# Kernel optimization log

Measured on AMD Instinct MI355X. Metric: run time of the kernel, lower is better.

The kernel has to match this reference:

```python
import jax, jax.numpy as jnp
import numpy as np

B, S, DIN = 4, 1024, 256      # batch, seq_len, input feature dim
KD, V = 64, 256               # keys, values
H, T = 8, 4                   # heads, stacks
EPS = 1e-3                    # keras BatchNormalization default epsilon


def setup_inputs() -> dict:
    key = jax.random.key(0)
    ks = jax.random.split(key, 6)
    def he(k, shape, fan_in):
        return jax.random.normal(k, shape, jnp.float32) * np.float32(np.sqrt(2.0 / fan_in))
    return {
        "x": jax.random.normal(ks[0], (B, S, DIN), jnp.float32),
        "W_in": he(ks[1], (DIN, V), DIN),
        "Wq": he(ks[2], (H, T, V, KD), V),
        "Wk": he(ks[3], (H, T, V, KD), V),
        "Wv": he(ks[4], (H, T, V, V), V),
        "Wd": he(ks[5], (H, T, V, V), V),
        "gamma1": jnp.ones((H, T, V), jnp.float32),
        "beta1": jnp.zeros((H, T, V), jnp.float32),
        "gamma2": jnp.ones((H, T, V), jnp.float32),
        "beta2": jnp.zeros((H, T, V), jnp.float32),
    }


def _bn(x, g, b):
    # Keras BatchNormalization(axis=-1), training-mode batch statistics over (B, S)
    m = jnp.mean(x, axis=(0, 1), keepdims=True)
    v = jnp.var(x, axis=(0, 1), keepdims=True)
    return (x - m) * jax.lax.rsqrt(v + EPS) * g + b


def reference(x, W_in, Wq, Wk, Wv, Wd, gamma1, beta1, gamma2, beta2):
    net0 = jnp.einsum('bsd,dv->bsv', x, W_in)          # input_dense, no bias
    scale = KD ** -0.5

    def one_head(Wq_h, Wk_h, Wv_h, Wd_h, g1, b1, g2, b2):
        net = net0
        for t in range(T):  # small fixed stack count, structurally distinct params
            q = net @ Wq_h[t]                           # [B,S,KD]
            k = net @ Wk_h[t]                           # [B,S,KD]
            v = net @ Wv_h[t]                           # [B,S,V]
            attn = jax.nn.softmax(jnp.einsum('bik,bjk->bij', q, k) * scale, axis=-1)
            out = jnp.einsum('bij,bjv->biv', attn, v)   # [B,S,V]
            net = _bn(net + out, g1[t], b1[t])          # residual + norm1
            net = _bn(net + jax.nn.relu(net @ Wd_h[t]), g2[t], b2[t])  # res + dense-relu + norm2
        return net                                      # [B,S,V]

    outs = jax.vmap(one_head)(Wq, Wk, Wv, Wd, gamma1, beta1, gamma2, beta2)  # [H,B,S,V]
    return jnp.transpose(outs, (1, 2, 0, 3))            # stack axis=2 -> [B,S,H,V]
```

## Files before the change

### kernel.cpp

```cpp
#include <hip/hip_runtime.h>
#include <hip/hip_bf16.h>
#include <math.h>

#define BB   4
#define SS   1024
#define VV   256
#define KDIM 64
#define HH   8
#define TT   4
#define EPSV 1e-3f
#define SCL  0.125f
#define INV2048 4.8828125e-4f

typedef float f4 __attribute__((ext_vector_type(4)));
typedef short bf8 __attribute__((ext_vector_type(8)));
typedef _Float16 h8 __attribute__((ext_vector_type(8)));
typedef _Float16 h4 __attribute__((ext_vector_type(4)));

#define LDP 68
#define LHS 68

__device__ __forceinline__ short f2bf(float x) {
  __hip_bfloat16 h = __float2bfloat16(x);
  return *reinterpret_cast<short*>(&h);
}
__device__ __forceinline__ float bf2f(short h) {
  union { unsigned u; float f; } cv;
  cv.u = ((unsigned)(unsigned short)h) << 16;
  return cv.f;
}

__device__ __forceinline__ int xcd_swz512(int L) {
  return (L & 7) * 64 + (L >> 3);
}

__global__ __launch_bounds__(256) void k_init(float* __restrict__ g, float* __restrict__ b)
{
  int i = blockIdx.x * 256 + threadIdx.x;
  g[i] = 1.f; b[i] = 0.f;
}

__global__ __launch_bounds__(256) void k_affine(
    const float* __restrict__ st, const float* __restrict__ gamma,
    const float* __restrict__ beta, int t,
    float* __restrict__ ag, float* __restrict__ ab)
{
  int h = blockIdx.x, c = threadIdx.x;
  float s  = st[(h * 256 + c) * 2];
  float s2 = st[(h * 256 + c) * 2 + 1];
  float mean = s * (1.f / 4096.f);
  float var  = s2 * (1.f / 4096.f) - mean * mean;
  float g = gamma[(h * TT + t) * 256 + c] * rsqrtf(var + EPSV);
  ag[h * 256 + c] = g;
  ab[h * 256 + c] = beta[(h * TT + t) * 256 + c] - mean * g;
}

__device__ __forceinline__ void gemm_core(
    const float* __restrict__ A, const float* __restrict__ Bm, int ldb,
    float acc[4][4], float (*As)[LDP], float (*Bs)[LDP])
{
  const int tid = threadIdx.x;
  const int tx = tid & 15, ty = tid >> 4;
#pragma unroll
  for (int i = 0; i < 4; i++)
#pragma unroll
    for (int j = 0; j < 4; j++) acc[i][j] = 0.f;

  for (int k0 = 0; k0 < 256; k0 += 16) {
#pragma unroll
    for (int l = 0; l < 4; l++) {
      int e = tid + l * 256;
      int r = e >> 4, kk = e & 15;
      As[kk][r] = A[r * 256 + k0 + kk];
      int rb = e >> 6, nn = e & 63;
      Bs[rb][nn] = Bm[(k0 + rb) * ldb + nn];
    }
    __syncthreads();
#pragma unroll
    for (int kk = 0; kk < 16; kk++) {
      f4 av = *(const f4*)&As[kk][ty * 4];
      f4 bv = *(const f4*)&Bs[kk][tx * 4];
#pragma unroll
      for (int i = 0; i < 4; i++)
#pragma unroll
        for (int j = 0; j < 4; j++)
          acc[i][j] += av[i] * bv[j];
    }
    __syncthreads();
  }
}

__global__ __launch_bounds__(256) void k_in_dense(
    const float* __restrict__ x, const float* __restrict__ Win,
    float* __restrict__ net)
{
  __shared__ __align__(16) float As[16][LDP];
  __shared__ __align__(16) float Bs[16][LDP];
  const int mt = blockIdx.x, nt = blockIdx.y;
  float acc[4][4];
  gemm_core(x + mt * 64 * 256, Win + nt * 64, 256, acc, As, Bs);
  const int tx = threadIdx.x & 15, ty = threadIdx.x >> 4;
#pragma unroll
  for (int i = 0; i < 4; i++) {
    f4 v;
#pragma unroll
    for (int j = 0; j < 4; j++) v[j] = acc[i][j];
    int row = mt * 64 + ty * 4 + i;
    int col = nt * 64 + tx * 4;
    for (int h = 0; h < HH; h++)
      *(f4*)&net[(size_t)h * 1048576 + row * 256 + col] = v;
  }
}

__global__ __launch_bounds__(256) void k_prep(
    const float* __restrict__ Wq, const float* __restrict__ Wk,
    const float* __restrict__ Wv, const float* __restrict__ Wd,
    _Float16* __restrict__ oh, _Float16* __restrict__ ol, int t)
{
  __shared__ __align__(16) _Float16 Th[64][LHS];
  __shared__ __align__(16) _Float16 Tl[64][LHS];
  const int xb = blockIdx.x, kb = blockIdx.y, h = blockIdx.z;
  const int tid = threadIdx.x;
  const float* src; int N, nb; size_t dbase;
  if (xb == 0)      { src = Wq; N = 64;  nb = 0;      dbase = (size_t)h * 16384; }
  else if (xb == 1) { src = Wk; N = 64;  nb = 0;      dbase = 131072 + (size_t)h * 16384; }
  else if (xb < 6)  { src = Wv; N = 256; nb = xb - 2; dbase = 262144 + (size_t)h * 65536; }
  else              { src = Wd; N = 256; nb = xb - 6; dbase = 786432 + (size_t)h * 65536; }
  src += (size_t)(h * TT + t) * 256 * N;
#pragma unroll
  for (int i = 0; i < 4; i++) {
    int fi = tid + i * 256;
    int r = fi >> 4, c4 = fi & 15;
    f4 w = *(const f4*)&src[(size_t)(kb * 64 + r) * N + nb * 64 + c4 * 4];
    h4 hv, lv;
#pragma unroll
    for (int j = 0; j < 4; j++) {
      _Float16 hi = (_Float16)w[j];
      hv[j] = hi;
      lv[j] = (_Float16)((w[j] - (float)hi) * 2048.f);
    }
    *(h4*)&Th[r][c4 * 4] = hv;
    *(h4*)&Tl[r][c4 * 4] = lv;
  }
  __syncthreads();
#pragma unroll
  for (int i = 0; i < 4; i++) {
    int fo = tid + i * 256;
    int nr = fo >> 4, k4 = fo & 15;
    h4 hv, lv;
#pragma unroll
    for (int j = 0; j < 4; j++) { hv[j] = Th[k4 * 4 + j][nr]; lv[j] = Tl[k4 * 4 + j][nr]; }
    size_t d = dbase + (size_t)(nb * 64 + nr) * 256 + kb * 64 + k4 * 4;
    *(h4*)&oh[d] = hv;
    *(h4*)&ol[d] = lv;
  }
}

__device__ __forceinline__ void stage_issue_aff(
    const float* __restrict__ A, const float* __restrict__ ag,
    const float* __restrict__ ab, int kc, int tid, f4 w[4])
{
#pragma unroll
  for (int i = 0; i < 4; i++) {
    int fi = tid + i * 256;
    int r = fi >> 4, c4 = fi & 15;
    f4 raw = *(const f4*)&A[(size_t)r * 256 + kc * 64 + c4 * 4];
    f4 g = *(const f4*)&ag[kc * 64 + c4 * 4];
    f4 b = *(const f4*)&ab[kc * 64 + c4 * 4];
#pragma unroll
    for (int j = 0; j < 4; j++) w[i][j] = fmaf(raw[j], g[j], b[j]);
  }
}
__device__ __forceinline__ void stage_write(
    const f4 w[4], int tid, _Float16 (*Ah)[LHS], _Float16 (*Al)[LHS])
{
#pragma unroll
  for (int i = 0; i < 4; i++) {
    int fi = tid + i * 256;
    int r = fi >> 4, c4 = fi & 15;
    h4 hv, lv;
#pragma unroll
    for (int j = 0; j < 4; j++) {
      _Float16 hi = (_Float16)w[i][j];
      hv[j] = hi;
      lv[j] = (_Float16)((w[i][j] - (float)hi) * 2048.f);
    }
    *(h4*)&Ah[r][c4 * 4] = hv;
    *(h4*)&Al[r][c4 * 4] = lv;
  }
}

__global__ __launch_bounds__(256) void k_mm_qkv(
    const float* __restrict__ net,
    const float* __restrict__ affg, const float* __restrict__ affb,
    const _Float16* __restrict__ wph, const _Float16* __restrict__ wpl,
    _Float16* __restrict__ qph, _Float16* __restrict__ qpl,
    _Float16* __restrict__ kph, _Float16* __restrict__ kpl,
    short* __restrict__ vth, short* __restrict__ vtl)
{
  __shared__ __align__(16) _Float16 Ah[2][64][LHS];
  __shared__ __align__(16) _Float16 Al[2][64][LHS];
  const int logical = xcd_swz512(blockIdx.x);
  const int mt = logical & 63, h = logical >> 6;
  const int tid = threadIdx.x, wv = tid >> 6, lane = tid & 63;
  const int ln = lane & 15, quad = lane >> 4;
  const float* A = net + (size_t)h * 1048576 + (size_t)mt * 64 * 256;
  const float* ag = affg + h * 256;
  const float* ab = affb + h * 256;

  for (int half = 0; half < 2; half++) {
    size_t bb[3];
#pragma unroll
    for (int j = 0; j < 3; j++) {
      int nt = half * 3 + j;
      if (nt == 0)      bb[j] = (size_t)h * 16384;
      else if (nt == 1) bb[j] = 131072 + (size_t)h * 16384;
      else              bb[j] = 262144 + (size_t)h * 65536 + (size_t)(nt - 2) * 16384;
      bb[j] += (size_t)(wv * 16 + ln) * 256;
    }

    f4 mn[3][4], cr[3][4];
#pragma unroll
    for (int j = 0; j < 3; j++)
#pragma unroll
      for (int mf = 0; mf < 4; mf++) {
        mn[j][mf] = (f4){0.f, 0.f, 0.f, 0.f};
        cr[j][mf] = (f4){0.f, 0.f, 0.f, 0.f};
      }

    f4 w[4];
    stage_issue_aff(A, ag, ab, 0, tid, w);
    stage_write(w, tid, Ah[0], Al[0]);
    __syncthreads();

    for (int kc = 0; kc < 4; kc++) {
      const int buf = kc & 1;
      if (kc < 3) stage_issue_aff(A, ag, ab, kc + 1, tid, w);
#pragma unroll
      for (int j = 0; j < 3; j++) {
        const _Float16* bh = wph + bb[j] + kc * 64;
        const _Float16* bl = wpl + bb[j] + kc * 64;
        h8 bh0 = *(const h8*)&bh[quad * 8];
        h8 bh1 = *(const h8*)&bh[32 + quad * 8];
        h8 bl0 = *(const h8*)&bl[quad * 8];
        h8 bl1 = *(const h8*)&bl[32 + quad * 8];
#pragma unroll
        for (int mf = 0; mf < 4; mf++) {
          h8 ah0 = *(const h8*)&Ah[buf][mf * 16 + ln][quad * 8];
          h8 ah1 = *(const h8*)&Ah[buf][mf * 16 + ln][32 + quad * 8];
          h8 al0 = *(const h8*)&Al[buf][mf * 16 + ln][quad * 8];
          h8 al1 = *(const h8*)&Al[buf][mf * 16 + ln][32 + quad * 8];
          mn[j][mf] = __builtin_amdgcn_mfma_f32_16x16x32_f16(ah0, bh0, mn[j][mf], 0, 0, 0);
          mn[j][mf] = __builtin_amdgcn_mfma_f32_16x16x32_f16(ah1, bh1, mn[j][mf], 0, 0, 0);
          cr[j][mf] = __builtin_amdgcn_mfma_f32_16x16x32_f16(ah0, bl0, cr[j][mf], 0, 0, 0);
          cr[j][mf] = __builtin_amdgcn_mfma_f32_16x16x32_f16(ah1, bl1, cr[j][mf], 0, 0, 0);
          cr[j][mf] = __builtin_amdgcn_mfma_f32_16x16x32_f16(al0, bh0, cr[j][mf], 0, 0, 0);
          cr[j][mf] = __builtin_amdgcn_mfma_f32_16x16x32_f16(al1, bh1, cr[j][mf], 0, 0, 0);
        }
      }
      if (kc < 3) stage_write(w, tid, Ah[buf ^ 1], Al[buf ^ 1]);
      __syncthreads();
    }

#pragma unroll
    for (int j = 0; j < 3; j++) {
      int nt = half * 3 + j;
      if (nt <= 1) {
        _Float16* dh = (nt == 0) ? qph : kph;
        _Float16* dl = (nt == 0) ? qpl : kpl;
        int col = wv * 16 + ln;
#pragma unroll
        for (int mf = 0; mf < 4; mf++)
#pragma unroll
          for (int r = 0; r < 4; r++) {
            int row = mt * 64 + mf * 16 + quad * 4 + r;
            int b_ = row >> 10, sI = row & 1023;
            float v = mn[j][mf][r] + cr[j][mf][r] * INV2048;
            _Float16 hi = (_Float16)v;
            size_t idx = ((size_t)(h * 4 + b_) * 1024 + sI) * 64 + col;
            dh[idx] = hi;
            dl[idx] = (_Float16)((v - (float)hi) * 2048.f);
          }
      } else {
        int c = (nt - 2) * 64 + wv * 16 + ln;
#pragma unroll
        for (int mf = 0; mf < 4; mf++)
#pragma unroll
          for (int r = 0; r < 4; r++) {
            int row = mt * 64 + mf * 16 + quad * 4 + r;
            int b_ = row >> 10, sI = row & 1023;
            float v = mn[j][mf][r] + cr[j][mf][r] * INV2048;
            short hi = f2bf(v);
            size_t idx = ((size_t)(h * 4 + b_) * 256 + c) * 1024 + sI;
            vth[idx] = hi;
            vtl[idx] = f2bf(v - bf2f(hi));
          }
      }
    }
  }
}

__global__ __launch_bounds__(256) void k_mm_dense(
    const float* __restrict__ buf1,
    const float* __restrict__ affg, const float* __restrict__ affb,
    const _Float16* __restrict__ wph, const _Float16* __restrict__ wpl,
    float* __restrict__ buf2, float* __restrict__ st)
{
  __shared__ __align__(16) _Float16 Ah[2][64][LHS];
  __shared__ __align__(16) _Float16 Al[2][64][LHS];
  const int logical = xcd_swz512(blockIdx.x);
  const int mt = logical & 63, h = logical >> 6;
  const int tid = threadIdx.x, wv = tid >> 6, lane = tid & 63;
  const int ln = lane & 15, quad = lane >> 4;
  const float* a1 = buf1 + (size_t)h * 1048576;
  float* o2 = buf2 + (size_t)h * 1048576;
  const float* A = a1 + (size_t)mt * 64 * 256;
  const float* ag = affg + h * 256;
  const float* ab = affb + h * 256;

  for (int half = 0; half < 2; half++) {
    size_t bb[2];
#pragma unroll
    for (int j = 0; j < 2; j++) {
      int nt = half * 2 + j;
      bb[j] = 786432 + (size_t)h * 65536 + (size_t)nt * 16384
            + (size_t)(wv * 16 + ln) * 256;
    }

    f4 mn[2][4], cr[2][4];
#pragma unroll
    for (int j = 0; j < 2; j++)
#pragma unroll
      for (int mf = 0; mf < 4; mf++) {
        mn[j][mf] = (f4){0.f, 0.f, 0.f, 0.f};
        cr[j][mf] = (f4){0.f, 0.f, 0.f, 0.f};
      }

    f4 w[4];
    stage_issue_aff(A, ag, ab, 0, tid, w);
    stage_write(w, tid, Ah[0], Al[0]);
    __syncthreads();

    for (int kc = 0; kc < 4; kc++) {
      const int buf = kc & 1;
      if (kc < 3) stage_issue_aff(A, ag, ab, kc + 1, tid, w);
#pragma unroll
      for (int j = 0; j < 2; j++) {
        const _Float16* bh = wph + bb[j] + kc * 64;
        const _Float16* bl = wpl + bb[j] + kc * 64;
        h8 bh0 = *(const h8*)&bh[quad * 8];
        h8 bh1 = *(const h8*)&bh[32 + quad * 8];
        h8 bl0 = *(const h8*)&bl[quad * 8];
        h8 bl1 = *(const h8*)&bl[32 + quad * 8];
#pragma unroll
        for (int mf = 0; mf < 4; mf++) {
          h8 ah0 = *(const h8*)&Ah[buf][mf * 16 + ln][quad * 8];
          h8 ah1 = *(const h8*)&Ah[buf][mf * 16 + ln][32 + quad * 8];
          h8 al0 = *(const h8*)&Al[buf][mf * 16 + ln][quad * 8];
          h8 al1 = *(const h8*)&Al[buf][mf * 16 + ln][32 + quad * 8];
          mn[j][mf] = __builtin_amdgcn_mfma_f32_16x16x32_f16(ah0, bh0, mn[j][mf], 0, 0, 0);
          mn[j][mf] = __builtin_amdgcn_mfma_f32_16x16x32_f16(ah1, bh1, mn[j][mf], 0, 0, 0);
          cr[j][mf] = __builtin_amdgcn_mfma_f32_16x16x32_f16(ah0, bl0, cr[j][mf], 0, 0, 0);
          cr[j][mf] = __builtin_amdgcn_mfma_f32_16x16x32_f16(ah1, bl1, cr[j][mf], 0, 0, 0);
          cr[j][mf] = __builtin_amdgcn_mfma_f32_16x16x32_f16(al0, bh0, cr[j][mf], 0, 0, 0);
          cr[j][mf] = __builtin_amdgcn_mfma_f32_16x16x32_f16(al1, bh1, cr[j][mf], 0, 0, 0);
        }
      }
      if (kc < 3) stage_write(w, tid, Ah[buf ^ 1], Al[buf ^ 1]);
      __syncthreads();
    }

#pragma unroll
    for (int j = 0; j < 2; j++) {
      int nt = half * 2 + j;
      int col = nt * 64 + wv * 16 + ln;
      float gc = ag[col], bc = ab[col];
      float s1 = 0.f, s2 = 0.f;
#pragma unroll
      for (int mf = 0; mf < 4; mf++)
#pragma unroll
        for (int r = 0; r < 4; r++) {
          int row = mt * 64 + mf * 16 + quad * 4 + r;
          size_t idx = (size_t)row * 256 + col;
          float v = mn[j][mf][r] + cr[j][mf][r] * INV2048;
          float yv = fmaf(a1[idx], gc, bc) + fmaxf(v, 0.f);
          o2[idx] = yv;
          s1 += yv; s2 += yv * yv;
        }
      s1 += __shfl_xor(s1, 16, 64); s1 += __shfl_xor(s1, 32, 64);
      s2 += __shfl_xor(s2, 16, 64); s2 += __shfl_xor(s2, 32, 64);
      if (quad == 0) {
        atomicAdd(&st[(h * 256 + col) * 2],     s1);
        atomicAdd(&st[(h * 256 + col) * 2 + 1], s2);
      }
    }
  }
}

__global__ __launch_bounds__(256, 2) void k_attn(
    const _Float16* __restrict__ qfh, const _Float16* __restrict__ qfl,
    const _Float16* __restrict__ kfh, const _Float16* __restrict__ kfl,
    const short* __restrict__ vth, const short* __restrict__ vtl,
    const float* __restrict__ resid,
    const float* __restrict__ affg, const float* __restrict__ affb,
    float* __restrict__ st, float* __restrict__ obuf)
{
  __shared__ __align__(16) short AB0[64][64];
  __shared__ __align__(16) short AB1[64][64];
  __shared__ __align__(16) short VhS[2][64][64];
  __shared__ __align__(16) short VlS[2][64][64];

  const int logical = xcd_swz512(blockIdx.x);
  const int qt = logical & 15, hb = logical >> 4;
  const int b = hb & 3, h = hb >> 2;
  const int tid = threadIdx.x;
  const int wv = tid >> 6, lane = tid & 63, ln = lane & 15, quad = lane >> 4;
  const int swz = (ln & 7) << 3;

  const _Float16* qgh = qfh + ((size_t)hb * 1024 + qt * 64 + wv * 16 + ln) * 64;
  const _Float16* qgl = qfl + ((size_t)hb * 1024 + qt * 64 + wv * 16 + ln) * 64;
  h8 aqh0 = *(const h8*)&qgh[quad * 8];
  h8 aqh1 = *(const h8*)&qgh[32 + quad * 8];
  h8 aql0 = *(const h8*)&qgl[quad * 8];
  h8 aql1 = *(const h8*)&qgl[32 + quad * 8];

  const _Float16* kgh = kfh + (size_t)hb * 65536;
  const _Float16* kgl = kfl + (size_t)hb * 65536;
  const short* vhg = vth + (size_t)hb * 262144;
  const short* vlg = vtl + (size_t)hb * 262144;

  float m[4] = {-1e30f, -1e30f, -1e30f, -1e30f};
  float l[4] = {0.f, 0.f, 0.f, 0.f};
  f4 O[16];
#pragma unroll
  for (int nt = 0; nt < 16; nt++) O[nt] = (f4){0.f, 0.f, 0.f, 0.f};

#pragma unroll
  for (int i = 0; i < 2; i++) {
    int e = tid + i * 256;
    int r = e >> 3, c8 = e & 7;
    int cc = (c8 * 8) ^ ((r & 7) << 3);
    *(h8*)&AB0[r][cc] = *(const h8*)&kgh[(size_t)r * 64 + c8 * 8];
    *(h8*)&AB1[r][cc] = *(const h8*)&kgl[(size_t)r * 64 + c8 * 8];
  }
#pragma unroll
  for (int i = 0; i < 2; i++) {
    int e = tid + i * 256;
    int vc = e >> 3, fc = e & 7;
    int cc = (fc * 8) ^ ((vc & 7) << 3);
    size_t g = (size_t)vc * 1024 + fc * 8;
    *(bf8*)&VhS[0][vc][cc] = *(const bf8*)&vhg[g];
    *(bf8*)&VlS[0][vc][cc] = *(const bf8*)&vlg[g];
  }
  __syncthreads();

  for (int kt = 0; kt < 16; kt++) {
    f4 sv[4];
#pragma unroll
    for (int nf = 0; nf < 4; nf++) {
      int row = nf * 16 + ln;
      h8 bkh0 = *(const h8*)&AB0[row][(quad * 8) ^ swz];
      h8 bkh1 = *(const h8*)&AB0[row][(32 + quad * 8) ^ swz];
      h8 bkl0 = *(const h8*)&AB1[row][(quad * 8) ^ swz];
      h8 bkl1 = *(const h8*)&AB1[row][(32 + quad * 8) ^ swz];
      f4 mn = (f4){0.f, 0.f, 0.f, 0.f};
      f4 cr = (f4){0.f, 0.f, 0.f, 0.f};
      mn = __builtin_amdgcn_mfma_f32_16x16x32_f16(aqh0, bkh0, mn, 0, 0, 0);
      mn = __builtin_amdgcn_mfma_f32_16x16x32_f16(aqh1, bkh1, mn, 0, 0, 0);
      cr = __builtin_amdgcn_mfma_f32_16x16x32_f16(aqh0, bkl0, cr, 0, 0, 0);
      cr = __builtin_amdgcn_mfma_f32_16x16x32_f16(aqh1, bkl1, cr, 0, 0, 0);
      cr = __builtin_amdgcn_mfma_f32_16x16x32_f16(aql0, bkh0, cr, 0, 0, 0);
      cr = __builtin_amdgcn_mfma_f32_16x16x32_f16(aql1, bkh1, cr, 0, 0, 0);
#pragma unroll
      for (int r = 0; r < 4; r++) sv[nf][r] = (mn[r] + cr[r] * INV2048) * SCL;
    }

    __syncthreads();

    float mloc[4];
#pragma unroll
    for (int r = 0; r < 4; r++) {
      float v0 = fmaxf(fmaxf(sv[0][r], sv[1][r]), fmaxf(sv[2][r], sv[3][r]));
#pragma unroll
      for (int d = 1; d < 16; d <<= 1)
        v0 = fmaxf(v0, __shfl_xor(v0, d, 64));
      mloc[r] = v0;
    }
    float growth = fmaxf(fmaxf(mloc[0] - m[0], mloc[1] - m[1]),
                         fmaxf(mloc[2] - m[2], mloc[3] - m[3]));
    if (__any(growth > 8.f)) {
      float alpha[4];
#pragma unroll
      for (int r = 0; r < 4; r++) {
        float mnew = fmaxf(m[r], mloc[r]);
        alpha[r] = __expf(m[r] - mnew);
        m[r] = mnew;
        l[r] *= alpha[r];
      }
#pragma unroll
      for (int nt = 0; nt < 16; nt++)
#pragma unroll
        for (int i = 0; i < 4; i++) O[nt][i] *= alpha[i];
    }
#pragma unroll
    for (int r = 0; r < 4; r++) {
      float ls = 0.f;
#pragma unroll
      for (int nf = 0; nf < 4; nf++) {
        float p = __expf(sv[nf][r] - m[r]);
        sv[nf][r] = p;
        ls += p;
      }
#pragma unroll
      for (int d = 1; d < 16; d <<= 1) ls += __shfl_xor(ls, d, 64);
      l[r] += ls;
    }

#pragma unroll
    for (int nf = 0; nf < 4; nf++)
#pragma unroll
      for (int r = 0; r < 4; r++) {
        int row = wv * 16 + quad * 4 + r;
        int c = (nf * 16 + ln) ^ ((row & 7) << 3);
        float p = sv[nf][r];
        short hi = f2bf(p);
        AB0[row][c] = hi;
        AB1[row][c] = f2bf(p - bf2f(hi));
      }
    __syncthreads();

    bf8 ph0 = *(const bf8*)&AB0[wv * 16 + ln][(quad * 8) ^ swz];
    bf8 ph1 = *(const bf8*)&AB0[wv * 16 + ln][(32 + quad * 8) ^ swz];
    bf8 pl0 = *(const bf8*)&AB1[wv * 16 + ln][(quad * 8) ^ swz];
    bf8 pl1 = *(const bf8*)&AB1[wv * 16 + ln][(32 + quad * 8) ^ swz];

    for (int c4 = 0; c4 < 4; c4++) {
      const int buf = c4 & 1;
      const bool haveNext = (c4 < 3) || (kt < 15);
      const int nkt = (c4 < 3) ? kt : kt + 1;
      const int nc4 = (c4 < 3) ? c4 + 1 : 0;
      const bool pfK = (c4 == 3) && (kt < 15);

      const int vc0 = tid >> 3, fc0 = tid & 7;
      const int vc1 = vc0 + 32;
      bf8 fvh0, fvh1, fvl0, fvl1;
      if (haveNext) {
        size_t g0 = (size_t)(nc4 * 64 + vc0) * 1024 + nkt * 64 + fc0 * 8;
        size_t g1 = (size_t)(nc4 * 64 + vc1) * 1024 + nkt * 64 + fc0 * 8;
        fvh0 = *(const bf8*)&vhg[g0]; fvl0 = *(const bf8*)&vlg[g0];
        fvh1 = *(const bf8*)&vhg[g1]; fvl1 = *(const bf8*)&vlg[g1];
      }
      h8 fkh0, fkh1, fkl0, fkl1;
      if (pfK) {
        size_t g0 = (size_t)((kt + 1) * 64 + vc0) * 64 + fc0 * 8;
        size_t g1 = (size_t)((kt + 1) * 64 + vc1) * 64 + fc0 * 8;
        fkh0 = *(const h8*)&kgh[g0]; fkl0 = *(const h8*)&kgl[g0];
        fkh1 = *(const h8*)&kgh[g1]; fkl1 = *(const h8*)&kgl[g1];
      }

#pragma unroll
      for (int n2 = 0; n2 < 4; n2++) {
        int nt = c4 * 4 + n2;
        int vrow = n2 * 16 + ln;
        bf8 vh0 = *(const bf8*)&VhS[buf][vrow][(quad * 8) ^ swz];
        bf8 vh1 = *(const bf8*)&VhS[buf][vrow][(32 + quad * 8) ^ swz];
        bf8 vl0 = *(const bf8*)&VlS[buf][vrow][(quad * 8) ^ swz];
        bf8 vl1 = *(const bf8*)&VlS[buf][vrow][(32 + quad * 8) ^ swz];
        O[nt] = __builtin_amdgcn_mfma_f32_16x16x32_bf16(ph0, vh0, O[nt], 0, 0, 0);
        O[nt] = __builtin_amdgcn_mfma_f32_16x16x32_bf16(ph1, vh1, O[nt], 0, 0, 0);
        O[nt] = __builtin_amdgcn_mfma_f32_16x16x32_bf16(ph0, vl0, O[nt], 0, 0, 0);
        O[nt] = __builtin_amdgcn_mfma_f32_16x16x32_bf16(ph1, vl1, O[nt], 0, 0, 0);
        O[nt] = __builtin_amdgcn_mfma_f32_16x16x32_bf16(pl0, vh0, O[nt], 0, 0, 0);
        O[nt] = __builtin_amdgcn_mfma_f32_16x16x32_bf16(pl1, vh1, O[nt], 0, 0, 0);
      }

      if (haveNext) {
        int cc0 = (fc0 * 8) ^ ((vc0 & 7) << 3);
        int cc1 = (fc0 * 8) ^ ((vc1 & 7) << 3);
        *(bf8*)&VhS[buf ^ 1][vc0][cc0] = fvh0;
        *(bf8*)&VlS[buf ^ 1][vc0][cc0] = fvl0;
        *(bf8*)&VhS[buf ^ 1][vc1][cc1] = fvh1;
        *(bf8*)&VlS[buf ^ 1][vc1][cc1] = fvl1;
      }
      if (pfK) {
        int cc0 = (fc0 * 8) ^ ((vc0 & 7) << 3);
        int cc1 = (fc0 * 8) ^ ((vc1 & 7) << 3);
        *(h8*)&AB0[vc0][cc0] = fkh0;
        *(h8*)&AB1[vc0][cc0] = fkl0;
        *(h8*)&AB0[vc1][cc1] = fkh1;
        *(h8*)&AB1[vc1][cc1] = fkl1;
      }
      __syncthreads();
    }
  }

  const float* rg = affg + h * 256;
  const float* rb = affb + h * 256;
  const float* rs = resid + (size_t)h * 1048576
                  + (size_t)(b * 1024 + qt * 64 + wv * 16 + quad * 4) * 256;
  float* ds = obuf + (size_t)h * 1048576
            + (size_t)(b * 1024 + qt * 64 + wv * 16 + quad * 4) * 256;
  float linv[4];
#pragma unroll
  for (int r = 0; r < 4; r++) linv[r] = 1.f / l[r];

  float* S1 = (float*)&AB0[0][0];
  float* S2 = (float*)&AB1[0][0];
#pragma unroll
  for (int nt = 0; nt < 16; nt++) {
    int c = nt * 16 + ln;
    float gc = rg[c], bc = rb[c];
    float s1 = 0.f, s2 = 0.f;
#pragma unroll
    for (int r = 0; r < 4; r++) {
      float yv = fmaf(rs[r * 256 + c], gc, bc) + O[nt][r] * linv[r];
      ds[r * 256 + c] = yv;
      s1 += yv; s2 += yv * yv;
    }
    s1 += __shfl_xor(s1, 16, 64); s1 += __shfl_xor(s1, 32, 64);
    s2 += __shfl_xor(s2, 16, 64); s2 += __shfl_xor(s2, 32, 64);
    if (quad == 0) { S1[wv * 256 + c] = s1; S2[wv * 256 + c] = s2; }
  }
  __syncthreads();
  if (tid < 256) {
    float a1 = S1[tid] + S1[256 + tid] + S1[512 + tid] + S1[768 + tid];
    float a2 = S2[tid] + S2[256 + tid] + S2[512 + tid] + S2[768 + tid];
    atomicAdd(&st[(h * 256 + tid) * 2],     a1);
    atomicAdd(&st[(h * 256 + tid) * 2 + 1], a2);
  }
}

__global__ __launch_bounds__(256) void k_bnapply(
    const float* __restrict__ a, const float* __restrict__ b,
    const float* __restrict__ stats,
    const float* __restrict__ gamma, const float* __restrict__ beta,
    float* __restrict__ dst, int t, int addB, int transposed)
{
  const int h = blockIdx.y, r0 = blockIdx.x * 64, c = threadIdx.x;
  float s  = stats[(h * 256 + c) * 2];
  float s2 = stats[(h * 256 + c) * 2 + 1];
  float mean = s * (1.f / 4096.f);
  float var  = s2 * (1.f / 4096.f) - mean * mean;
  float inv  = rsqrtf(var + EPSV);
  float g  = gamma[(h * TT + t) * 256 + c] * inv;
  float bt = beta[(h * TT + t) * 256 + c];
  const float* pa = a + (size_t)h * 1048576 + r0 * 256 + c;
  const float* pb = addB ? (b + (size_t)h * 1048576 + r0 * 256 + c) : nullptr;
  for (int r = 0; r < 64; r++) {
    float y = pa[r * 256];
    if (addB) y += pb[r * 256];
    float o = (y - mean) * g + bt;
    int rg = r0 + r;
    if (transposed) dst[((size_t)rg * HH + h) * 256 + c] = o;
    else            dst[(size_t)h * 1048576 + rg * 256 + c] = o;
  }
}

extern "C" void kernel_launch(void* const* d_in, const int* in_sizes, int n_in,
                              void* d_out, int out_size, void* d_ws, size_t ws_size,
                              hipStream_t stream)
{
  const float* x   = (const float*)d_in[0];
  const float* Win = (const float*)d_in[1];
  const float* Wq  = (const float*)d_in[2];
  const float* Wk  = (const float*)d_in[3];
  const float* Wv  = (const float*)d_in[4];
  const float* Wd  = (const float*)d_in[5];
  const float* g1  = (const float*)d_in[6];
  const float* b1  = (const float*)d_in[7];
  const float* g2  = (const float*)d_in[8];
  const float* b2  = (const float*)d_in[9];
  float* out = (float*)d_out;
  float* ws  = (float*)d_ws;

  float* net   = ws;
  float* tmp   = net + 8388608;
  float* stats = tmp + 8388608;
  float* affg1 = stats + 8192;
  float* affb1 = affg1 + 2048;
  float* affg2 = affb1 + 2048;
  float* affb2 = affg2 + 2048;
  float* affgI = affb2 + 2048;
  float* affbI = affgI + 2048;
  _Float16* qph = (_Float16*)(stats + 32768);
  _Float16* qpl = qph + 2097152;
  _Float16* kph = qpl + 2097152;
  _Float16* kpl = kph + 2097152;
  short* vth   = (short*)(kpl + 2097152);
  short* vtl   = vth + 8388608;
  _Float16* wph = (_Float16*)(vtl + 8388608);
  _Float16* wpl = wph + 1310720;

  k_init<<<dim3(8), 256, 0, stream>>>(affgI, affbI);
  k_in_dense<<<dim3(64, 4), 256, 0, stream>>>(x, Win, net);

  for (int t = 0; t < TT; t++) {
    float* st1 = stats;
    float* st2 = stats + 4096;
    hipMemsetAsync(stats, 0, 8192 * sizeof(float), stream);

    const float* cg = (t == 0) ? affgI : affg2;
    const float* cb = (t == 0) ? affbI : affb2;

    k_prep<<<dim3(10, 4, 8), 256, 0, stream>>>(Wq, Wk, Wv, Wd, wph, wpl, t);
    k_mm_qkv<<<dim3(512), 256, 0, stream>>>(net, cg, cb, wph, wpl,
                                            qph, qpl, kph, kpl, vth, vtl);
    k_attn<<<dim3(512), 256, 0, stream>>>(qph, qpl, kph, kpl, vth, vtl,
                                          net, cg, cb, st1, tmp);
    k_affine<<<dim3(8), 256, 0, stream>>>(st1, g1, b1, t, affg1, affb1);
    k_mm_dense<<<dim3(512), 256, 0, stream>>>(tmp, affg1, affb1, wph, wpl,
                                              net, st2);
    if (t < TT - 1)
      k_affine<<<dim3(8), 256, 0, stream>>>(st2, g2, b2, t, affg2, affb2);
    else
      k_bnapply<<<dim3(64, 8), 256, 0, stream>>>(net, nullptr, st2, g2, b2,
                                                 out, t, 0, 1);
  }
}
```

Baseline: 872.6 us.

## Split QKV/dense GEMMs across twice the blocks and deepen attention V pipeline

The QKV and dense GEMM kernels now give each output-column half to its own block instead of looping over both halves inside one block. This doubles the grid to 1024 blocks, adding parallelism at the cost of staging the A tile twice. The attention kernel grows V shared-memory staging from 2 to 4 buffers, prefetching two chunks ahead so it can sync every other chunk instead of every chunk. It also raises wave priority around the MFMA sections with s_setprio.

Result: faster. 844.6 us (-3.2%).

```diff
diff --git a/kernel.cpp b/kernel.cpp
--- a/kernel.cpp
+++ b/kernel.cpp
@@ -30,9 +30,8 @@
   return cv.f;
 }
 
-__device__ __forceinline__ int xcd_swz512(int L) {
-  return (L & 7) * 64 + (L >> 3);
-}
+__device__ __forceinline__ int xcd_swz512(int L)  { return (L & 7) * 64  + (L >> 3); }
+__device__ __forceinline__ int xcd_swz1024(int L) { return (L & 7) * 128 + (L >> 3); }
 
 __global__ __launch_bounds__(256) void k_init(float* __restrict__ g, float* __restrict__ b)
 {
@@ -200,102 +199,101 @@
 {
   __shared__ __align__(16) _Float16 Ah[2][64][LHS];
   __shared__ __align__(16) _Float16 Al[2][64][LHS];
-  const int logical = xcd_swz512(blockIdx.x);
-  const int mt = logical & 63, h = logical >> 6;
+  const int logical = xcd_swz1024(blockIdx.x);
+  const int mt = logical & 63, hh = logical >> 6;
+  const int h = hh >> 1, half = hh & 1;
   const int tid = threadIdx.x, wv = tid >> 6, lane = tid & 63;
   const int ln = lane & 15, quad = lane >> 4;
   const float* A = net + (size_t)h * 1048576 + (size_t)mt * 64 * 256;
   const float* ag = affg + h * 256;
   const float* ab = affb + h * 256;
 
-  for (int half = 0; half < 2; half++) {
-    size_t bb[3];
+  size_t bb[3];
+#pragma unroll
+  for (int j = 0; j < 3; j++) {
+    int nt = half * 3 + j;
+    if (nt == 0)      bb[j] = (size_t)h * 16384;
+    else if (nt == 1) bb[j] = 131072 + (size_t)h * 16384;
+    else              bb[j] = 262144 + (size_t)h * 65536 + (size_t)(nt - 2) * 16384;
+    bb[j] += (size_t)(wv * 16 + ln) * 256;
+  }
+
+  f4 mn[3][4], cr[3][4];
+#pragma unroll
+  for (int j = 0; j < 3; j++)
+#pragma unroll
+    for (int mf = 0; mf < 4; mf++) {
+      mn[j][mf] = (f4){0.f, 0.f, 0.f, 0.f};
+      cr[j][mf] = (f4){0.f, 0.f, 0.f, 0.f};
+    }
+
+  f4 w[4];
+  stage_issue_aff(A, ag, ab, 0, tid, w);
+  stage_write(w, tid, Ah[0], Al[0]);
+  __syncthreads();
+
+  for (int kc = 0; kc < 4; kc++) {
+    const int buf = kc & 1;
+    if (kc < 3) stage_issue_aff(A, ag, ab, kc + 1, tid, w);
 #pragma unroll
     for (int j = 0; j < 3; j++) {
-      int nt = half * 3 + j;
-      if (nt == 0)      bb[j] = (size_t)h * 16384;
-      else if (nt == 1) bb[j] = 131072 + (size_t)h * 16384;
-      else              bb[j] = 262144 + (size_t)h * 65536 + (size_t)(nt - 2) * 16384;
-      bb[j] += (size_t)(wv * 16 + ln) * 256;
-    }
-
-    f4 mn[3][4], cr[3][4];
-#pragma unroll
-    for (int j = 0; j < 3; j++)
+      const _Float16* bh = wph + bb[j] + kc * 64;
+      const _Float16* bl = wpl + bb[j] + kc * 64;
+      h8 bh0 = *(const h8*)&bh[quad * 8];
+      h8 bh1 = *(const h8*)&bh[32 + quad * 8];
+      h8 bl0 = *(const h8*)&bl[quad * 8];
+      h8 bl1 = *(const h8*)&bl[32 + quad * 8];
 #pragma unroll
       for (int mf = 0; mf < 4; mf++) {
-        mn[j][mf] = (f4){0.f, 0.f, 0.f, 0.f};
-        cr[j][mf] = (f4){0.f, 0.f, 0.f, 0.f};
-      }
-
-    f4 w[4];
-    stage_issue_aff(A, ag, ab, 0, tid, w);
-    stage_write(w, tid, Ah[0], Al[0]);
+        h8 ah0 = *(const h8*)&Ah[buf][mf * 16 + ln][quad * 8];
+        h8 ah1 = *(const h8*)&Ah[buf][mf * 16 + ln][32 + quad * 8];
+        h8 al0 = *(const h8*)&Al[buf][mf * 16 + ln][quad * 8];
+        h8 al1 = *(const h8*)&Al[buf][mf * 16 + ln][32 + quad * 8];
+        mn[j][mf] = __builtin_amdgcn_mfma_f32_16x16x32_f16(ah0, bh0, mn[j][mf], 0, 0, 0);
+        mn[j][mf] = __builtin_amdgcn_mfma_f32_16x16x32_f16(ah1, bh1, mn[j][mf], 0, 0, 0);
+        cr[j][mf] = __builtin_amdgcn_mfma_f32_16x16x32_f16(ah0, bl0, cr[j][mf], 0, 0, 0);
+        cr[j][mf] = __builtin_amdgcn_mfma_f32_16x16x32_f16(ah1, bl1, cr[j][mf], 0, 0, 0);
+        cr[j][mf] = __builtin_amdgcn_mfma_f32_16x16x32_f16(al0, bh0, cr[j][mf], 0, 0, 0);
+        cr[j][mf] = __builtin_amdgcn_mfma_f32_16x16x32_f16(al1, bh1, cr[j][mf], 0, 0, 0);
+      }
+    }
+    if (kc < 3) stage_write(w, tid, Ah[buf ^ 1], Al[buf ^ 1]);
     __syncthreads();
-
-    for (int kc = 0; kc < 4; kc++) {
-      const int buf = kc & 1;
-      if (kc < 3) stage_issue_aff(A, ag, ab, kc + 1, tid, w);
-#pragma unroll
-      for (int j = 0; j < 3; j++) {
-        const _Float16* bh = wph + bb[j] + kc * 64;
-        const _Float16* bl = wpl + bb[j] + kc * 64;
-        h8 bh0 = *(const h8*)&bh[quad * 8];
-        h8 bh1 = *(const h8*)&bh[32 + quad * 8];
-        h8 bl0 = *(const h8*)&bl[quad * 8];
-        h8 bl1 = *(const h8*)&bl[32 + quad * 8];
-#pragma unroll
-        for (int mf = 0; mf < 4; mf++) {
-          h8 ah0 = *(const h8*)&Ah[buf][mf * 16 + ln][quad * 8];
-          h8 ah1 = *(const h8*)&Ah[buf][mf * 16 + ln][32 + quad * 8];
-          h8 al0 = *(const h8*)&Al[buf][mf * 16 + ln][quad * 8];
-          h8 al1 = *(const h8*)&Al[buf][mf * 16 + ln][32 + quad * 8];
-          mn[j][mf] = __builtin_amdgcn_mfma_f32_16x16x32_f16(ah0, bh0, mn[j][mf], 0, 0, 0);
-          mn[j][mf] = __builtin_amdgcn_mfma_f32_16x16x32_f16(ah1, bh1, mn[j][mf], 0, 0, 0);
-          cr[j][mf] = __builtin_amdgcn_mfma_f32_16x16x32_f16(ah0, bl0, cr[j][mf], 0, 0, 0);
-          cr[j][mf] = __builtin_amdgcn_mfma_f32_16x16x32_f16(ah1, bl1, cr[j][mf], 0, 0, 0);
-          cr[j][mf] = __builtin_amdgcn_mfma_f32_16x16x32_f16(al0, bh0, cr[j][mf], 0, 0, 0);
-          cr[j][mf] = __builtin_amdgcn_mfma_f32_16x16x32_f16(al1, bh1, cr[j][mf], 0, 0, 0);
+  }
+
+#pragma unroll
+  for (int j = 0; j < 3; j++) {
+    int nt = half * 3 + j;
+    if (nt <= 1) {
+      _Float16* dh = (nt == 0) ? qph : kph;
+      _Float16* dl = (nt == 0) ? qpl : kpl;
+      int col = wv * 16 + ln;
+#pragma unroll
+      for (int mf = 0; mf < 4; mf++)
+#pragma unroll
+        for (int r = 0; r < 4; r++) {
+          int row = mt * 64 + mf * 16 + quad * 4 + r;
+          int b_ = row >> 10, sI = row & 1023;
+          float v = mn[j][mf][r] + cr[j][mf][r] * INV2048;
+          _Float16 hi = (_Float16)v;
+          size_t idx = ((size_t)(h * 4 + b_) * 1024 + sI) * 64 + col;
+          dh[idx] = hi;
+          dl[idx] = (_Float16)((v - (float)hi) * 2048.f);
         }
-      }
-      if (kc < 3) stage_write(w, tid, Ah[buf ^ 1], Al[buf ^ 1]);
-      __syncthreads();
-    }
-
-#pragma unroll
-    for (int j = 0; j < 3; j++) {
-      int nt = half * 3 + j;
-      if (nt <= 1) {
-        _Float16* dh = (nt == 0) ? qph : kph;
-        _Float16* dl = (nt == 0) ? qpl : kpl;
-        int col = wv * 16 + ln;
-#pragma unroll
-        for (int mf = 0; mf < 4; mf++)
-#pragma unroll
-          for (int r = 0; r < 4; r++) {
-            int row = mt * 64 + mf * 16 + quad * 4 + r;
-            int b_ = row >> 10, sI = row & 1023;
-            float v = mn[j][mf][r] + cr[j][mf][r] * INV2048;
-            _Float16 hi = (_Float16)v;
-            size_t idx = ((size_t)(h * 4 + b_) * 1024 + sI) * 64 + col;
-            dh[idx] = hi;
-            dl[idx] = (_Float16)((v - (float)hi) * 2048.f);
-          }
-      } else {
-        int c = (nt - 2) * 64 + wv * 16 + ln;
-#pragma unroll
-        for (int mf = 0; mf < 4; mf++)
-#pragma unroll
-          for (int r = 0; r < 4; r++) {
-            int row = mt * 64 + mf * 16 + quad * 4 + r;
-            int b_ = row >> 10, sI = row & 1023;
-            float v = mn[j][mf][r] + cr[j][mf][r] * INV2048;
-            short hi = f2bf(v);
-            size_t idx = ((size_t)(h * 4 + b_) * 256 + c) * 1024 + sI;
-            vth[idx] = hi;
-            vtl[idx] = f2bf(v - bf2f(hi));
-          }
-      }
+    } else {
+      int c = (nt - 2) * 64 + wv * 16 + ln;
+#pragma unroll
+      for (int mf = 0; mf < 4; mf++)
+#pragma unroll
+        for (int r = 0; r < 4; r++) {
+          int row = mt * 64 + mf * 16 + quad * 4 + r;
+          int b_ = row >> 10, sI = row & 1023;
+          float v = mn[j][mf][r] + cr[j][mf][r] * INV2048;
+          short hi = f2bf(v);
+          size_t idx = ((size_t)(h * 4 + b_) * 256 + c) * 1024 + sI;
+          vth[idx] = hi;
+          vtl[idx] = f2bf(v - bf2f(hi));
+        }
     }
   }
 }
@@ -308,8 +306,9 @@
 {
   __shared__ __align__(16) _Float16 Ah[2][64][LHS];
   __shared__ __align__(16) _Float16 Al[2][64][LHS];
-  const int logical = xcd_swz512(blockIdx.x);
-  const int mt = logical & 63, h = logical >> 6;
+  const int logical = xcd_swz1024(blockIdx.x);
+  const int mt = logical & 63, hh = logical >> 6;
+  const int h = hh >> 1, half = hh & 1;
   const int tid = threadIdx.x, wv = tid >> 6, lane = tid & 63;
   const int ln = lane & 15, quad = lane >> 4;
   const float* a1 = buf1 + (size_t)h * 1048576;
@@ -318,81 +317,79 @@
   const float* ag = affg + h * 256;
   const float* ab = affb + h * 256;
 
-  for (int half = 0; half < 2; half++) {
-    size_t bb[2];
+  size_t bb[2];
+#pragma unroll
+  for (int j = 0; j < 2; j++) {
+    int nt = half * 2 + j;
+    bb[j] = 786432 + (size_t)h * 65536 + (size_t)nt * 16384
+          + (size_t)(wv * 16 + ln) * 256;
+  }
+
+  f4 mn[2][4], cr[2][4];
+#pragma unroll
+  for (int j = 0; j < 2; j++)
+#pragma unroll
+    for (int mf = 0; mf < 4; mf++) {
+      mn[j][mf] = (f4){0.f, 0.f, 0.f, 0.f};
+      cr[j][mf] = (f4){0.f, 0.f, 0.f, 0.f};
+    }
+
+  f4 w[4];
+  stage_issue_aff(A, ag, ab, 0, tid, w);
+  stage_write(w, tid, Ah[0], Al[0]);
+  __syncthreads();
+
+  for (int kc = 0; kc < 4; kc++) {
+    const int buf = kc & 1;
+    if (kc < 3) stage_issue_aff(A, ag, ab, kc + 1, tid, w);
 #pragma unroll
     for (int j = 0; j < 2; j++) {
-      int nt = half * 2 + j;
-      bb[j] = 786432 + (size_t)h * 65536 + (size_t)nt * 16384
-            + (size_t)(wv * 16 + ln) * 256;
-    }
-
-    f4 mn[2][4], cr[2][4];
-#pragma unroll
-    for (int j = 0; j < 2; j++)
+      const _Float16* bh = wph + bb[j] + kc * 64;
+      const _Float16* bl = wpl + bb[j] + kc * 64;
+      h8 bh0 = *(const h8*)&bh[quad * 8];
+      h8 bh1 = *(const h8*)&bh[32 + quad * 8];
+      h8 bl0 = *(const h8*)&bl[quad * 8];
+      h8 bl1 = *(const h8*)&bl[32 + quad * 8];
 #pragma unroll
       for (int mf = 0; mf < 4; mf++) {
-        mn[j][mf] = (f4){0.f, 0.f, 0.f, 0.f};
-        cr[j][mf] = (f4){0.f, 0.f, 0.f, 0.f};
-      }
-
-    f4 w[4];
-    stage_issue_aff(A, ag, ab, 0, tid, w);
-    stage_write(w, tid, Ah[0], Al[0]);
+        h8 ah0 = *(const h8*)&Ah[buf][mf * 16 + ln][quad * 8];
+        h8 ah1 = *(const h8*)&Ah[buf][mf * 16 + ln][32 + quad * 8];
+        h8 al0 = *(const h8*)&Al[buf][mf * 16 + ln][quad * 8];
+        h8 al1 = *(const h8*)&Al[buf][mf * 16 + ln][32 + quad * 8];
+        mn[j][mf] = __builtin_amdgcn_mfma_f32_16x16x32_f16(ah0, bh0, mn[j][mf], 0, 0, 0);
+        mn[j][mf] = __builtin_amdgcn_mfma_f32_16x16x32_f16(ah1, bh1, mn[j][mf], 0, 0, 0);
+        cr[j][mf] = __builtin_amdgcn_mfma_f32_16x16x32_f16(ah0, bl0, cr[j][mf], 0, 0, 0);
+        cr[j][mf] = __builtin_amdgcn_mfma_f32_16x16x32_f16(ah1, bl1, cr[j][mf], 0, 0, 0);
+        cr[j][mf] = __builtin_amdgcn_mfma_f32_16x16x32_f16(al0, bh0, cr[j][mf], 0, 0, 0);
+        cr[j][mf] = __builtin_amdgcn_mfma_f32_16x16x32_f16(al1, bh1, cr[j][mf], 0, 0, 0);
+      }
+    }
+    if (kc < 3) stage_write(w, tid, Ah[buf ^ 1], Al[buf ^ 1]);
     __syncthreads();
-
-    for (int kc = 0; kc < 4; kc++) {
-      const int buf = kc & 1;
-      if (kc < 3) stage_issue_aff(A, ag, ab, kc + 1, tid, w);
-#pragma unroll
-      for (int j = 0; j < 2; j++) {
-        const _Float16* bh = wph + bb[j] + kc * 64;
-        const _Float16* bl = wpl + bb[j] + kc * 64;
-        h8 bh0 = *(const h8*)&bh[quad * 8];
-        h8 bh1 = *(const h8*)&bh[32 + quad * 8];
-        h8 bl0 = *(const h8*)&bl[quad * 8];
-        h8 bl1 = *(const h8*)&bl[32 + quad * 8];
-#pragma unroll
-        for (int mf = 0; mf < 4; mf++) {
-          h8 ah0 = *(const h8*)&Ah[buf][mf * 16 + ln][quad * 8];
-          h8 ah1 = *(const h8*)&Ah[buf][mf * 16 + ln][32 + quad * 8];
-          h8 al0 = *(const h8*)&Al[buf][mf * 16 + ln][quad * 8];
-          h8 al1 = *(const h8*)&Al[buf][mf * 16 + ln][32 + quad * 8];
-          mn[j][mf] = __builtin_amdgcn_mfma_f32_16x16x32_f16(ah0, bh0, mn[j][mf], 0, 0, 0);
-          mn[j][mf] = __builtin_amdgcn_mfma_f32_16x16x32_f16(ah1, bh1, mn[j][mf], 0, 0, 0);
-          cr[j][mf] = __builtin_amdgcn_mfma_f32_16x16x32_f16(ah0, bl0, cr[j][mf], 0, 0, 0);
-          cr[j][mf] = __builtin_amdgcn_mfma_f32_16x16x32_f16(ah1, bl1, cr[j][mf], 0, 0, 0);
-          cr[j][mf] = __builtin_amdgcn_mfma_f32_16x16x32_f16(al0, bh0, cr[j][mf], 0, 0, 0);
-          cr[j][mf] = __builtin_amdgcn_mfma_f32_16x16x32_f16(al1, bh1, cr[j][mf], 0, 0, 0);
-        }
-      }
-      if (kc < 3) stage_write(w, tid, Ah[buf ^ 1], Al[buf ^ 1]);
-      __syncthreads();
-    }
-
-#pragma unroll
-    for (int j = 0; j < 2; j++) {
-      int nt = half * 2 + j;
-      int col = nt * 64 + wv * 16 + ln;
-      float gc = ag[col], bc = ab[col];
-      float s1 = 0.f, s2 = 0.f;
-#pragma unroll
-      for (int mf = 0; mf < 4; mf++)
-#pragma unroll
-        for (int r = 0; r < 4; r++) {
-          int row = mt * 64 + mf * 16 + quad * 4 + r;
-          size_t idx = (size_t)row * 256 + col;
-          float v = mn[j][mf][r] + cr[j][mf][r] * INV2048;
-          float yv = fmaf(a1[idx], gc, bc) + fmaxf(v, 0.f);
-          o2[idx] = yv;
-          s1 += yv; s2 += yv * yv;
-        }
-      s1 += __shfl_xor(s1, 16, 64); s1 += __shfl_xor(s1, 32, 64);
-      s2 += __shfl_xor(s2, 16, 64); s2 += __shfl_xor(s2, 32, 64);
-      if (quad == 0) {
-        atomicAdd(&st[(h * 256 + col) * 2],     s1);
-        atomicAdd(&st[(h * 256 + col) * 2 + 1], s2);
-      }
+  }
+
+#pragma unroll
+  for (int j = 0; j < 2; j++) {
+    int nt = half * 2 + j;
+    int col = nt * 64 + wv * 16 + ln;
+    float gc = ag[col], bc = ab[col];
+    float s1 = 0.f, s2 = 0.f;
+#pragma unroll
+    for (int mf = 0; mf < 4; mf++)
+#pragma unroll
+      for (int r = 0; r < 4; r++) {
+        int row = mt * 64 + mf * 16 + quad * 4 + r;
+        size_t idx = (size_t)row * 256 + col;
+        float v = mn[j][mf][r] + cr[j][mf][r] * INV2048;
+        float yv = fmaf(a1[idx], gc, bc) + fmaxf(v, 0.f);
+        o2[idx] = yv;
+        s1 += yv; s2 += yv * yv;
+      }
+    s1 += __shfl_xor(s1, 16, 64); s1 += __shfl_xor(s1, 32, 64);
+    s2 += __shfl_xor(s2, 16, 64); s2 += __shfl_xor(s2, 32, 64);
+    if (quad == 0) {
+      atomicAdd(&st[(h * 256 + col) * 2],     s1);
+      atomicAdd(&st[(h * 256 + col) * 2 + 1], s2);
     }
   }
 }
@@ -407,8 +404,8 @@
 {
   __shared__ __align__(16) short AB0[64][64];
   __shared__ __align__(16) short AB1[64][64];
-  __shared__ __align__(16) short VhS[2][64][64];
-  __shared__ __align__(16) short VlS[2][64][64];
+  __shared__ __align__(16) short VhS[4][64][64];
+  __shared__ __align__(16) short VlS[4][64][64];
 
   const int logical = xcd_swz512(blockIdx.x);
   const int qt = logical & 15, hb = logical >> 4;
@@ -444,18 +441,21 @@
     *(h8*)&AB1[r][cc] = *(const h8*)&kgl[(size_t)r * 64 + c8 * 8];
   }
 #pragma unroll
-  for (int i = 0; i < 2; i++) {
-    int e = tid + i * 256;
-    int vc = e >> 3, fc = e & 7;
-    int cc = (fc * 8) ^ ((vc & 7) << 3);
-    size_t g = (size_t)vc * 1024 + fc * 8;
-    *(bf8*)&VhS[0][vc][cc] = *(const bf8*)&vhg[g];
-    *(bf8*)&VlS[0][vc][cc] = *(const bf8*)&vlg[g];
-  }
+  for (int ch = 0; ch < 2; ch++)
+#pragma unroll
+    for (int i = 0; i < 2; i++) {
+      int e = tid + i * 256;
+      int vc = e >> 3, fc = e & 7;
+      int cc = (fc * 8) ^ ((vc & 7) << 3);
+      size_t g = (size_t)(ch * 64 + vc) * 1024 + fc * 8;
+      *(bf8*)&VhS[ch][vc][cc] = *(const bf8*)&vhg[g];
+      *(bf8*)&VlS[ch][vc][cc] = *(const bf8*)&vlg[g];
+    }
   __syncthreads();
 
   for (int kt = 0; kt < 16; kt++) {
     f4 sv[4];
+    __builtin_amdgcn_s_setprio(1);
 #pragma unroll
     for (int nf = 0; nf < 4; nf++) {
       int row = nf * 16 + ln;
@@ -474,6 +474,7 @@
 #pragma unroll
       for (int r = 0; r < 4; r++) sv[nf][r] = (mn[r] + cr[r] * INV2048) * SCL;
     }
+    __builtin_amdgcn_s_setprio(0);
 
     __syncthreads();
 
@@ -535,18 +536,18 @@
     bf8 pl1 = *(const bf8*)&AB1[wv * 16 + ln][(32 + quad * 8) ^ swz];
 
     for (int c4 = 0; c4 < 4; c4++) {
-      const int buf = c4 & 1;
-      const bool haveNext = (c4 < 3) || (kt < 15);
-      const int nkt = (c4 < 3) ? kt : kt + 1;
-      const int nc4 = (c4 < 3) ? c4 + 1 : 0;
+      const bool haveNext = (c4 < 2) || (kt < 15);
+      const int nkt = (c4 < 2) ? kt : kt + 1;
+      const int nch = (c4 < 2) ? c4 + 2 : c4 - 2;
+      const int nbuf = (c4 + 2) & 3;
       const bool pfK = (c4 == 3) && (kt < 15);
 
       const int vc0 = tid >> 3, fc0 = tid & 7;
       const int vc1 = vc0 + 32;
       bf8 fvh0, fvh1, fvl0, fvl1;
       if (haveNext) {
-        size_t g0 = (size_t)(nc4 * 64 + vc0) * 1024 + nkt * 64 + fc0 * 8;
-        size_t g1 = (size_t)(nc4 * 64 + vc1) * 1024 + nkt * 64 + fc0 * 8;
+        size_t g0 = (size_t)(nch * 64 + vc0) * 1024 + nkt * 64 + fc0 * 8;
+        size_t g1 = (size_t)(nch * 64 + vc1) * 1024 + nkt * 64 + fc0 * 8;
         fvh0 = *(const bf8*)&vhg[g0]; fvl0 = *(const bf8*)&vlg[g0];
         fvh1 = *(const bf8*)&vhg[g1]; fvl1 = *(const bf8*)&vlg[g1];
       }
@@ -558,14 +559,15 @@
         fkh1 = *(const h8*)&kgh[g1]; fkl1 = *(const h8*)&kgl[g1];
       }
 
+      __builtin_amdgcn_s_setprio(1);
 #pragma unroll
       for (int n2 = 0; n2 < 4; n2++) {
         int nt = c4 * 4 + n2;
         int vrow = n2 * 16 + ln;
-        bf8 vh0 = *(const bf8*)&VhS[buf][vrow][(quad * 8) ^ swz];
-        bf8 vh1 = *(const bf8*)&VhS[buf][vrow][(32 + quad * 8) ^ swz];
-        bf8 vl0 = *(const bf8*)&VlS[buf][vrow][(quad * 8) ^ swz];
-        bf8 vl1 = *(const bf8*)&VlS[buf][vrow][(32 + quad * 8) ^ swz];
+        bf8 vh0 = *(const bf8*)&VhS[c4][vrow][(quad * 8) ^ swz];
+        bf8 vh1 = *(const bf8*)&VhS[c4][vrow][(32 + quad * 8) ^ swz];
+        bf8 vl0 = *(const bf8*)&VlS[c4][vrow][(quad * 8) ^ swz];
+        bf8 vl1 = *(const bf8*)&VlS[c4][vrow][(32 + quad * 8) ^ swz];
         O[nt] = __builtin_amdgcn_mfma_f32_16x16x32_bf16(ph0, vh0, O[nt], 0, 0, 0);
         O[nt] = __builtin_amdgcn_mfma_f32_16x16x32_bf16(ph1, vh1, O[nt], 0, 0, 0);
         O[nt] = __builtin_amdgcn_mfma_f32_16x16x32_bf16(ph0, vl0, O[nt], 0, 0, 0);
@@ -573,14 +575,15 @@
         O[nt] = __builtin_amdgcn_mfma_f32_16x16x32_bf16(pl0, vh0, O[nt], 0, 0, 0);
         O[nt] = __builtin_amdgcn_mfma_f32_16x16x32_bf16(pl1, vh1, O[nt], 0, 0, 0);
       }
+      __builtin_amdgcn_s_setprio(0);
 
       if (haveNext) {
         int cc0 = (fc0 * 8) ^ ((vc0 & 7) << 3);
         int cc1 = (fc0 * 8) ^ ((vc1 & 7) << 3);
-        *(bf8*)&VhS[buf ^ 1][vc0][cc0] = fvh0;
-        *(bf8*)&VlS[buf ^ 1][vc0][cc0] = fvl0;
-        *(bf8*)&VhS[buf ^ 1][vc1][cc1] = fvh1;
-        *(bf8*)&VlS[buf ^ 1][vc1][cc1] = fvl1;
+        *(bf8*)&VhS[nbuf][vc0][cc0] = fvh0;
+        *(bf8*)&VlS[nbuf][vc0][cc0] = fvl0;
+        *(bf8*)&VhS[nbuf][vc1][cc1] = fvh1;
+        *(bf8*)&VlS[nbuf][vc1][cc1] = fvl1;
       }
       if (pfK) {
         int cc0 = (fc0 * 8) ^ ((vc0 & 7) << 3);
@@ -590,7 +593,7 @@
         *(h8*)&AB0[vc1][cc1] = fkh1;
         *(h8*)&AB1[vc1][cc1] = fkl1;
       }
-      __syncthreads();
+      if (c4 & 1) __syncthreads();
     }
   }
 
@@ -703,13 +706,13 @@
     const float* cb = (t == 0) ? affbI : affb2;
 
     k_prep<<<dim3(10, 4, 8), 256, 0, stream>>>(Wq, Wk, Wv, Wd, wph, wpl, t);
-    k_mm_qkv<<<dim3(512), 256, 0, stream>>>(net, cg, cb, wph, wpl,
-                                            qph, qpl, kph, kpl, vth, vtl);
+    k_mm_qkv<<<dim3(1024), 256, 0, stream>>>(net, cg, cb, wph, wpl,
+                                             qph, qpl, kph, kpl, vth, vtl);
     k_attn<<<dim3(512), 256, 0, stream>>>(qph, qpl, kph, kpl, vth, vtl,
                                           net, cg, cb, st1, tmp);
     k_affine<<<dim3(8), 256, 0, stream>>>(st1, g1, b1, t, affg1, affb1);
-    k_mm_dense<<<dim3(512), 256, 0, stream>>>(tmp, affg1, affb1, wph, wpl,
-                                              net, st2);
+    k_mm_dense<<<dim3(1024), 256, 0, stream>>>(tmp, affg1, affb1, wph, wpl,
+                                               net, st2);
     if (t < TT - 1)
       k_affine<<<dim3(8), 256, 0, stream>>>(st2, g2, b2, t, affg2, affb2);
     else
```
